# Performance work log

Hardware: AMD Instinct MI355X
Metric: run time of the kernel (lower is better)

The kernel has to match this reference:

```python
import jax, jax.numpy as jnp
import numpy as np

N_NODES = 100000
N_EDGES = 1200000
N_GRAPHS = 256
IN_C, HID_C, OUT_C = 5, 64, 2


def gcn_conv(x, src, dst, W, b, n_nodes):
    """PyG GCNConv: h = x@W; add self-loops; deg from target col (edge weight 1);
    norm = deg^{-1/2}[src]*deg^{-1/2}[dst]; scatter-add messages into dst; + bias."""
    loop = jnp.arange(n_nodes, dtype=src.dtype)
    s = jnp.concatenate([src, loop])
    d = jnp.concatenate([dst, loop])
    deg = jax.ops.segment_sum(jnp.ones_like(d, dtype=x.dtype), d, num_segments=n_nodes)
    dinv = jnp.where(deg > 0, jax.lax.rsqrt(deg), 0.0)
    norm = dinv[s] * dinv[d]                     # [E+N]
    h = x @ W                                    # [N, out]
    msg = h[s] * norm[:, None]                   # gather + scale  [E+N, out]
    out = jax.ops.segment_sum(msg, d, num_segments=n_nodes)  # scatter-add
    return out + b


def setup_inputs() -> dict:
    key = jax.random.key(0)
    ks = jax.random.split(key, 10)
    x = jax.random.normal(ks[0], (N_NODES, IN_C), dtype=jnp.float32)
    edge_index = jax.random.randint(ks[1], (2, N_EDGES), 0, N_NODES, dtype=jnp.int64)
    batch = jnp.sort(jax.random.randint(ks[2], (N_NODES,), 0, N_GRAPHS, dtype=jnp.int64))
    def glorot(k, fan_in, fan_out):
        lim = np.sqrt(6.0 / (fan_in + fan_out))
        return jax.random.uniform(k, (fan_in, fan_out), jnp.float32, -lim, lim)
    W1 = glorot(ks[3], IN_C, HID_C)
    b1 = jnp.zeros((HID_C,), jnp.float32)
    W2 = glorot(ks[4], HID_C, HID_C)
    b2 = jnp.zeros((HID_C,), jnp.float32)
    Wfc = glorot(ks[5], HID_C, OUT_C)
    bfc = jnp.zeros((OUT_C,), jnp.float32)
    return {"x": x, "edge_index": edge_index, "batch": batch,
            "W1": W1, "b1": b1, "W2": W2, "b2": b2, "Wfc": Wfc, "bfc": bfc}


def reference(x, edge_index, batch, W1, b1, W2, b2, Wfc, bfc):
    src, dst = edge_index[0], edge_index[1]
    h = jax.nn.relu(gcn_conv(x, src, dst, W1, b1, N_NODES))
    h = jax.nn.relu(gcn_conv(h, src, dst, W2, b2, N_NODES))
    # global_mean_pool over graph ids in `batch`
    sums = jax.ops.segment_sum(h, batch, num_segments=N_GRAPHS)          # [G, H]
    cnts = jax.ops.segment_sum(jnp.ones((h.shape[0],), h.dtype), batch,
                               num_segments=N_GRAPHS)                    # [G]
    pooled = sums / jnp.maximum(cnts, 1.0)[:, None]
    return pooled @ Wfc + bfc                                            # [G, 2]
```

## Files before the change

### kernel.cpp

```cpp
#include <hip/hip_runtime.h>

#define N_NODES 100000
#define N_EDGES 1200000
#define N_GRAPHS 256
#define IN_C 5
#define HID_C 64
#define OUT_C 2

#define BSH 7
#define BNODES 128
#define NB ((N_NODES + BNODES - 1) / BNODES)
#define CAPB 2048
#define EPB 2048
#define NBLK_E ((N_EDGES + EPB - 1) / EPB)
#define GNPW 8
#define G1NPW 4

typedef unsigned int uint32;

__device__ __forceinline__ uint32 f2bf(float f) {
    uint32 x = __float_as_uint(f);
    return (x + 0x7FFFu + ((x >> 16) & 1u)) >> 16;
}
__device__ __forceinline__ float bflo(uint32 r) { return __uint_as_float(r << 16); }
__device__ __forceinline__ float bfhi(uint32 r) { return __uint_as_float(r & 0xFFFF0000u); }

__global__ void k_bscatter(const int* __restrict__ src, const int* __restrict__ dst,
                           int* __restrict__ bcnt, int* __restrict__ pairs) {
    __shared__ int h[NB];
    for (int i = threadIdx.x; i < NB; i += blockDim.x) h[i] = 0;
    __syncthreads();
    int e0 = blockIdx.x * EPB;
    int e1 = e0 + EPB; if (e1 > N_EDGES) e1 = N_EDGES;
    for (int e = e0 + threadIdx.x; e < e1; e += blockDim.x)
        atomicAdd(&h[dst[e] >> BSH], 1);
    __syncthreads();
    for (int i = threadIdx.x; i < NB; i += blockDim.x)
        if (h[i]) h[i] = (i << 11) + atomicAdd(&bcnt[i], h[i]);
    __syncthreads();
    for (int e = e0 + threadIdx.x; e < e1; e += blockDim.x) {
        int d = dst[e];
        int pos = atomicAdd(&h[d >> BSH], 1);
        pairs[pos] = ((d & (BNODES - 1)) << 17) | src[e];
    }
}

__global__ void k_bsort_g1(const int* __restrict__ pairs, const int* __restrict__ bcnt,
                           const float* __restrict__ x, const float* __restrict__ W1,
                           int* __restrict__ csr, int* __restrict__ rs,
                           int* __restrict__ cnt, float* __restrict__ dinv,
                           uint32* __restrict__ g) {
    __shared__ int hist[BNODES];
    __shared__ int tmp[BNODES];
    __shared__ int cur[BNODES];
    __shared__ float sdv[BNODES];
    __shared__ __align__(16) float sW1[IN_C * HID_C];
    __shared__ float sx[BNODES * IN_C];
    int b = blockIdx.x;
    int t = threadIdx.x;
    int base = b << BSH;
    if (t < BNODES) hist[t] = 0;
    for (int i = t; i < IN_C * HID_C; i += 256) sW1[i] = W1[i];
    for (int i = t; i < BNODES * IN_C; i += 256) {
        int gi = base * IN_C + i;
        sx[i] = (gi < N_NODES * IN_C) ? x[gi] : 0.f;
    }
    __syncthreads();
    int s = b << 11;
    int n = bcnt[b];
    for (int i = t; i < n; i += 256)
        atomicAdd(&hist[pairs[s + i] >> 17], 1);
    __syncthreads();
    int v = (t < BNODES) ? hist[t] : 0;
    if (t < BNODES) tmp[t] = v;
    __syncthreads();
    for (int off = 1; off < BNODES; off <<= 1) {
        int a = (t < BNODES && t >= off) ? tmp[t - off] : 0;
        __syncthreads();
        if (t < BNODES) tmp[t] += a;
        __syncthreads();
    }
    float dv_t = rsqrtf((float)v + 1.0f);
    if (t < BNODES) {
        cur[t] = tmp[t] - v;
        sdv[t] = dv_t;
        if (base + t < N_NODES) {
            rs[base + t] = s + tmp[t] - v;
            cnt[base + t] = v;
            dinv[base + t] = dv_t;
        }
    }
    __syncthreads();
    for (int i = t; i < n; i += 256) {
        int p = pairs[s + i];
        int pos = atomicAdd(&cur[p >> 17], 1);
        csr[s + pos] = p & 0x1FFFF;
    }
    for (int idx = t; idx < BNODES * 32; idx += 256) {
        int nl = idx >> 5, c2 = idx & 31;
        int node = base + nl;
        if (node >= N_NODES) break;
        float s0 = 0.f, s1 = 0.f;
#pragma unroll
        for (int k = 0; k < IN_C; ++k) {
            float xv = sx[nl * IN_C + k];
            float2 wv = *(const float2*)&sW1[k * HID_C + 2 * c2];
            s0 += xv * wv.x;
            s1 += xv * wv.y;
        }
        float dv = sdv[nl];
        g[(unsigned)node * 32 + c2] = (f2bf(s1 * dv) << 16) | f2bf(s0 * dv);
    }
}

__global__ void __launch_bounds__(256) k_gather_g2(
        const uint32* __restrict__ g1t, const int* __restrict__ csr,
        const int* __restrict__ rs, const int* __restrict__ cnt,
        const float* __restrict__ dinv, const float* __restrict__ b1,
        const float* __restrict__ W2, uint32* __restrict__ g2t) {
    __shared__ __align__(16) float sW2[HID_C * HID_C];
    __shared__ float srow[4][HID_C];
    int tid = threadIdx.x;
    for (int i = tid; i < HID_C * HID_C; i += 256) sW2[i] = W2[i];
    __syncthreads();
    int w = tid >> 6;
    int wv = __builtin_amdgcn_readfirstlane(blockIdx.x * 4 + w);
    int n0 = wv * G1NPW;
    if (n0 >= N_NODES) return;
    int n1 = n0 + G1NPW; if (n1 > N_NODES) n1 = N_NODES;
    int lane = tid & 63;
    int half = lane >> 5;
    int c2 = lane & 31;
    float bias0 = b1[2 * c2], bias1 = b1[2 * c2 + 1];
    for (int v = n0; v < n1; ++v) {
        int k0 = rs[v];
        int n = cnt[v];
        float s0 = 0.f, s1 = 0.f;
        if (half == 0) {
            uint32 r = g1t[(unsigned)v * 32 + c2];
            s0 = bflo(r); s1 = bfhi(r);
        }
        int i = 0;
        for (; i + 7 < n; i += 8) {
            int u0 = csr[k0 + i + 0], u1 = csr[k0 + i + 1];
            int u2 = csr[k0 + i + 2], u3 = csr[k0 + i + 3];
            int u4 = csr[k0 + i + 4], u5 = csr[k0 + i + 5];
            int u6 = csr[k0 + i + 6], u7 = csr[k0 + i + 7];
            int a0 = half ? u1 : u0;
            int a1 = half ? u3 : u2;
            int a2 = half ? u5 : u4;
            int a3 = half ? u7 : u6;
            uint32 r0 = g1t[(unsigned)a0 * 32 + c2];
            uint32 r1 = g1t[(unsigned)a1 * 32 + c2];
            uint32 r2 = g1t[(unsigned)a2 * 32 + c2];
            uint32 r3 = g1t[(unsigned)a3 * 32 + c2];
            s0 += (bflo(r0) + bflo(r1)) + (bflo(r2) + bflo(r3));
            s1 += (bfhi(r0) + bfhi(r1)) + (bfhi(r2) + bfhi(r3));
        }
        for (; i + 1 < n; i += 2) {
            int u0 = csr[k0 + i], u1 = csr[k0 + i + 1];
            int a = half ? u1 : u0;
            uint32 r = g1t[(unsigned)a * 32 + c2];
            s0 += bflo(r); s1 += bfhi(r);
        }
        if (i < n && half == 0) {
            uint32 r = g1t[(unsigned)csr[k0 + i] * 32 + c2];
            s0 += bflo(r); s1 += bfhi(r);
        }
        s0 += __shfl_xor(s0, 32);
        s1 += __shfl_xor(s1, 32);
        float dv = dinv[v];
        float o0 = fmaxf(s0 * dv + bias0, 0.f);
        float o1 = fmaxf(s1 * dv + bias1, 0.f);
        if (half == 0) *(float2*)&srow[w][2 * c2] = make_float2(o0, o1);
        int kb = half << 5;
        float a0 = 0.f, a1 = 0.f;
#pragma unroll 8
        for (int j = 0; j < 32; ++j) {
            float hv = srow[w][kb + j];
            float2 wvv = *(const float2*)&sW2[(kb + j) * HID_C + 2 * c2];
            a0 += hv * wvv.x;
            a1 += hv * wvv.y;
        }
        a0 += __shfl_xor(a0, 32);
        a1 += __shfl_xor(a1, 32);
        if (half == 0)
            g2t[(unsigned)v * 32 + c2] = (f2bf(a1 * dv) << 16) | f2bf(a0 * dv);
    }
}

__global__ void k_gather2p(const uint32* __restrict__ g, const int* __restrict__ csr,
                           const int* __restrict__ rs, const int* __restrict__ cnt,
                           const float* __restrict__ dinv, const float* __restrict__ b,
                           const int* __restrict__ batch, float* __restrict__ pooled) {
    int wv = __builtin_amdgcn_readfirstlane(
        blockIdx.x * (blockDim.x >> 6) + (threadIdx.x >> 6));
    int n0 = wv * GNPW;
    if (n0 >= N_NODES) return;
    int n1 = n0 + GNPW; if (n1 > N_NODES) n1 = N_NODES;
    int lane = threadIdx.x & 63;
    int half = lane >> 5;
    int c2 = lane & 31;
    float bias0 = b[2 * c2], bias1 = b[2 * c2 + 1];
    float p0 = 0.f, p1 = 0.f;
    int curg = batch[n0];
    for (int v = n0; v < n1; ++v) {
        int k0 = rs[v];
        int n = cnt[v];
        float s0 = 0.f, s1 = 0.f;
        if (half == 0) {
            uint32 r = g[(unsigned)v * 32 + c2];
            s0 = bflo(r); s1 = bfhi(r);
        }
        int i = 0;
        for (; i + 7 < n; i += 8) {
            int u0 = csr[k0 + i + 0], u1 = csr[k0 + i + 1];
            int u2 = csr[k0 + i + 2], u3 = csr[k0 + i + 3];
            int u4 = csr[k0 + i + 4], u5 = csr[k0 + i + 5];
            int u6 = csr[k0 + i + 6], u7 = csr[k0 + i + 7];
            int a0 = half ? u1 : u0;
            int a1 = half ? u3 : u2;
            int a2 = half ? u5 : u4;
            int a3 = half ? u7 : u6;
            uint32 r0 = g[(unsigned)a0 * 32 + c2];
            uint32 r1 = g[(unsigned)a1 * 32 + c2];
            uint32 r2 = g[(unsigned)a2 * 32 + c2];
            uint32 r3 = g[(unsigned)a3 * 32 + c2];
            s0 += (bflo(r0) + bflo(r1)) + (bflo(r2) + bflo(r3));
            s1 += (bfhi(r0) + bfhi(r1)) + (bfhi(r2) + bfhi(r3));
        }
        for (; i + 1 < n; i += 2) {
            int u0 = csr[k0 + i], u1 = csr[k0 + i + 1];
            int a = half ? u1 : u0;
            uint32 r = g[(unsigned)a * 32 + c2];
            s0 += bflo(r); s1 += bfhi(r);
        }
        if (i < n && half == 0) {
            uint32 r = g[(unsigned)csr[k0 + i] * 32 + c2];
            s0 += bflo(r); s1 += bfhi(r);
        }
        s0 += __shfl_xor(s0, 32);
        s1 += __shfl_xor(s1, 32);
        float dv = dinv[v];
        float o0 = fmaxf(s0 * dv + bias0, 0.f);
        float o1 = fmaxf(s1 * dv + bias1, 0.f);
        int gg = batch[v];
        if (gg != curg) {
            if (half == 0) {
                atomicAdd(&pooled[curg * HID_C + 2 * c2], p0);
                atomicAdd(&pooled[curg * HID_C + 2 * c2 + 1], p1);
            }
            p0 = 0.f; p1 = 0.f; curg = gg;
        }
        p0 += o0; p1 += o1;
    }
    if (half == 0) {
        atomicAdd(&pooled[curg * HID_C + 2 * c2], p0);
        atomicAdd(&pooled[curg * HID_C + 2 * c2 + 1], p1);
    }
}

__global__ void k_fc(const float* __restrict__ pooled, const int* __restrict__ batch,
                     const float* __restrict__ Wfc, const float* __restrict__ bfc,
                     float* __restrict__ out) {
    int g = blockIdx.x;
    int c = threadIdx.x;
    int lo = 0, hi = N_NODES;
    while (lo < hi) { int mid = (lo + hi) >> 1; if (batch[mid] < g) lo = mid + 1; else hi = mid; }
    int start = lo;
    hi = N_NODES;
    while (lo < hi) { int mid = (lo + hi) >> 1; if (batch[mid] < g + 1) lo = mid + 1; else hi = mid; }
    int n = lo - start;
    float pv = pooled[g * HID_C + c] / (float)(n > 0 ? n : 1);
    float o0 = pv * Wfc[c * OUT_C + 0];
    float o1 = pv * Wfc[c * OUT_C + 1];
#pragma unroll
    for (int off = 32; off > 0; off >>= 1) {
        o0 += __shfl_down(o0, off);
        o1 += __shfl_down(o1, off);
    }
    if (c == 0) {
        out[g * OUT_C + 0] = o0 + bfc[0];
        out[g * OUT_C + 1] = o1 + bfc[1];
    }
}

extern "C" void kernel_launch(void* const* d_in, const int* in_sizes, int n_in,
                              void* d_out, int out_size, void* d_ws, size_t ws_size,
                              hipStream_t stream) {
    const float* x    = (const float*)d_in[0];
    const int*   ei   = (const int*)d_in[1];
    const int*   src  = ei;
    const int*   dst  = ei + N_EDGES;
    const int*   batch= (const int*)d_in[2];
    const float* W1   = (const float*)d_in[3];
    const float* b1   = (const float*)d_in[4];
    const float* W2   = (const float*)d_in[5];
    const float* b2   = (const float*)d_in[6];
    const float* Wfc  = (const float*)d_in[7];
    const float* bfc  = (const float*)d_in[8];
    float* out = (float*)d_out;

    float*  ws     = (float*)d_ws;
    int*    bcnt   = (int*)ws;
    float*  pooled = ws + 1024;
    float*  dinv   = pooled + 16384;
    int*    cnt    = (int*)(dinv + 100352);
    int*    rs     = cnt + 100352;
    int*    pairs  = rs + 100352;
    int*    csr    = pairs + (NB * CAPB);
    uint32* g1tab  = (uint32*)(csr + (NB * CAPB));
    uint32* g2tab  = g1tab + N_NODES * 32;

    hipMemsetAsync(bcnt, 0, (1024 + 16384) * sizeof(float), stream);

    k_bscatter<<<NBLK_E, 256, 0, stream>>>(src, dst, bcnt, pairs);
    k_bsort_g1<<<NB, 256, 0, stream>>>(pairs, bcnt, x, W1, csr, rs, cnt, dinv, g1tab);

    {
        int waves = (N_NODES + G1NPW - 1) / G1NPW;
        int blocks = (waves + 3) / 4;
        k_gather_g2<<<blocks, 256, 0, stream>>>(g1tab, csr, rs, cnt, dinv, b1, W2, g2tab);
    }

    {
        int waves = (N_NODES + GNPW - 1) / GNPW;
        int blocks = (waves + 3) / 4;
        k_gather2p<<<blocks, 256, 0, stream>>>(g2tab, csr, rs, cnt, dinv, b2, batch, pooled);
    }

    k_fc<<<N_GRAPHS, 64, 0, stream>>>(pooled, batch, Wfc, bfc, out);
}
```

Before: 222.7 us.

## Pad CSR rows to multiples of four with self-loop and zero sentinel, vectorize gathers

Each CSR row now holds the self-loop and is padded to a multiple of four entries with a sentinel node whose feature row is zero. The gather kernels can then load four indices with one int4 load and have each quarter-wave fetch a uint2 (4 bf16 channels) per neighbor, with no scalar tail loops. The per-bucket CSR capacity is doubled to hold the padding. This removes tail handling and halves the number of feature-load instructions, at the cost of extra sentinel loads, more CSR memory traffic and an added shuffle reduction stage.

```diff
diff --git a/kernel.cpp b/kernel.cpp
--- a/kernel.cpp
+++ b/kernel.cpp
@@ -10,11 +10,13 @@
 #define BSH 7
 #define BNODES 128
 #define NB ((N_NODES + BNODES - 1) / BNODES)
-#define CAPB 2048
+#define CSH 12
+#define CAPB 4096
 #define EPB 2048
 #define NBLK_E ((N_EDGES + EPB - 1) / EPB)
 #define GNPW 8
 #define G1NPW 4
+#define SENT N_NODES
 
 typedef unsigned int uint32;
 
@@ -36,7 +38,7 @@
         atomicAdd(&h[dst[e] >> BSH], 1);
     __syncthreads();
     for (int i = threadIdx.x; i < NB; i += blockDim.x)
-        if (h[i]) h[i] = (i << 11) + atomicAdd(&bcnt[i], h[i]);
+        if (h[i]) h[i] = (i << CSH) + atomicAdd(&bcnt[i], h[i]);
     __syncthreads();
     for (int e = e0 + threadIdx.x; e < e1; e += blockDim.x) {
         int d = dst[e];
@@ -65,14 +67,16 @@
         int gi = base * IN_C + i;
         sx[i] = (gi < N_NODES * IN_C) ? x[gi] : 0.f;
     }
-    __syncthreads();
-    int s = b << 11;
+    if (b == 0 && t < 32) g[(unsigned)SENT * 32 + t] = 0u;
+    __syncthreads();
+    int s = b << CSH;
     int n = bcnt[b];
     for (int i = t; i < n; i += 256)
         atomicAdd(&hist[pairs[s + i] >> 17], 1);
     __syncthreads();
     int v = (t < BNODES) ? hist[t] : 0;
-    if (t < BNODES) tmp[t] = v;
+    int M = (v + 4) & ~3;
+    if (t < BNODES) tmp[t] = M;
     __syncthreads();
     for (int off = 1; off < BNODES; off <<= 1) {
         int a = (t < BNODES && t >= off) ? tmp[t - off] : 0;
@@ -82,11 +86,11 @@
     }
     float dv_t = rsqrtf((float)v + 1.0f);
     if (t < BNODES) {
-        cur[t] = tmp[t] - v;
+        cur[t] = tmp[t] - M;
         sdv[t] = dv_t;
         if (base + t < N_NODES) {
-            rs[base + t] = s + tmp[t] - v;
-            cnt[base + t] = v;
+            rs[base + t] = s + tmp[t] - M;
+            cnt[base + t] = M;
             dinv[base + t] = dv_t;
         }
     }
@@ -95,6 +99,13 @@
         int p = pairs[s + i];
         int pos = atomicAdd(&cur[p >> 17], 1);
         csr[s + pos] = p & 0x1FFFF;
+    }
+    __syncthreads();
+    if (t < BNODES && base + t < N_NODES) {
+        int p0 = cur[t];
+        int pe = tmp[t];
+        csr[s + p0] = base + t;
+        for (int j = p0 + 1; j < pe; ++j) csr[s + j] = SENT;
     }
     for (int idx = t; idx < BNODES * 32; idx += 256) {
         int nl = idx >> 5, c2 = idx & 31;
@@ -122,6 +133,7 @@
     __shared__ float srow[4][HID_C];
     int tid = threadIdx.x;
     for (int i = tid; i < HID_C * HID_C; i += 256) sW2[i] = W2[i];
+    if (blockIdx.x == 0 && tid < 32) g2t[(unsigned)SENT * 32 + tid] = 0u;
     __syncthreads();
     int w = tid >> 6;
     int wv = __builtin_amdgcn_readfirstlane(blockIdx.x * 4 + w);
@@ -129,50 +141,44 @@
     if (n0 >= N_NODES) return;
     int n1 = n0 + G1NPW; if (n1 > N_NODES) n1 = N_NODES;
     int lane = tid & 63;
+    int q = lane >> 4;
+    int c4 = lane & 15;
     int half = lane >> 5;
     int c2 = lane & 31;
-    float bias0 = b1[2 * c2], bias1 = b1[2 * c2 + 1];
+    float4 bia = *(const float4*)&b1[4 * c4];
     for (int v = n0; v < n1; ++v) {
         int k0 = rs[v];
-        int n = cnt[v];
-        float s0 = 0.f, s1 = 0.f;
-        if (half == 0) {
-            uint32 r = g1t[(unsigned)v * 32 + c2];
-            s0 = bflo(r); s1 = bfhi(r);
-        }
+        int M = cnt[v];
+        float s0 = 0.f, s1 = 0.f, s2 = 0.f, s3 = 0.f;
         int i = 0;
-        for (; i + 7 < n; i += 8) {
-            int u0 = csr[k0 + i + 0], u1 = csr[k0 + i + 1];
-            int u2 = csr[k0 + i + 2], u3 = csr[k0 + i + 3];
-            int u4 = csr[k0 + i + 4], u5 = csr[k0 + i + 5];
-            int u6 = csr[k0 + i + 6], u7 = csr[k0 + i + 7];
-            int a0 = half ? u1 : u0;
-            int a1 = half ? u3 : u2;
-            int a2 = half ? u5 : u4;
-            int a3 = half ? u7 : u6;
-            uint32 r0 = g1t[(unsigned)a0 * 32 + c2];
-            uint32 r1 = g1t[(unsigned)a1 * 32 + c2];
-            uint32 r2 = g1t[(unsigned)a2 * 32 + c2];
-            uint32 r3 = g1t[(unsigned)a3 * 32 + c2];
-            s0 += (bflo(r0) + bflo(r1)) + (bflo(r2) + bflo(r3));
-            s1 += (bfhi(r0) + bfhi(r1)) + (bfhi(r2) + bfhi(r3));
-        }
-        for (; i + 1 < n; i += 2) {
-            int u0 = csr[k0 + i], u1 = csr[k0 + i + 1];
-            int a = half ? u1 : u0;
-            uint32 r = g1t[(unsigned)a * 32 + c2];
-            s0 += bflo(r); s1 += bfhi(r);
-        }
-        if (i < n && half == 0) {
-            uint32 r = g1t[(unsigned)csr[k0 + i] * 32 + c2];
-            s0 += bflo(r); s1 += bfhi(r);
-        }
-        s0 += __shfl_xor(s0, 32);
-        s1 += __shfl_xor(s1, 32);
+        for (; i + 8 <= M; i += 8) {
+            int4 ua = *(const int4*)&csr[k0 + i];
+            int4 ub = *(const int4*)&csr[k0 + i + 4];
+            int a0 = (q == 0) ? ua.x : (q == 1) ? ua.y : (q == 2) ? ua.z : ua.w;
+            int a1 = (q == 0) ? ub.x : (q == 1) ? ub.y : (q == 2) ? ub.z : ub.w;
+            uint2 r0 = *(const uint2*)&g1t[(unsigned)a0 * 32 + 2 * c4];
+            uint2 r1 = *(const uint2*)&g1t[(unsigned)a1 * 32 + 2 * c4];
+            s0 += bflo(r0.x) + bflo(r1.x);
+            s1 += bfhi(r0.x) + bfhi(r1.x);
+            s2 += bflo(r0.y) + bflo(r1.y);
+            s3 += bfhi(r0.y) + bfhi(r1.y);
+        }
+        if (i < M) {
+            int4 ua = *(const int4*)&csr[k0 + i];
+            int a0 = (q == 0) ? ua.x : (q == 1) ? ua.y : (q == 2) ? ua.z : ua.w;
+            uint2 r0 = *(const uint2*)&g1t[(unsigned)a0 * 32 + 2 * c4];
+            s0 += bflo(r0.x); s1 += bfhi(r0.x); s2 += bflo(r0.y); s3 += bfhi(r0.y);
+        }
+        s0 += __shfl_xor(s0, 16); s1 += __shfl_xor(s1, 16);
+        s2 += __shfl_xor(s2, 16); s3 += __shfl_xor(s3, 16);
+        s0 += __shfl_xor(s0, 32); s1 += __shfl_xor(s1, 32);
+        s2 += __shfl_xor(s2, 32); s3 += __shfl_xor(s3, 32);
         float dv = dinv[v];
-        float o0 = fmaxf(s0 * dv + bias0, 0.f);
-        float o1 = fmaxf(s1 * dv + bias1, 0.f);
-        if (half == 0) *(float2*)&srow[w][2 * c2] = make_float2(o0, o1);
+        float o0 = fmaxf(s0 * dv + bia.x, 0.f);
+        float o1 = fmaxf(s1 * dv + bia.y, 0.f);
+        float o2 = fmaxf(s2 * dv + bia.z, 0.f);
+        float o3 = fmaxf(s3 * dv + bia.w, 0.f);
+        if (lane < 16) *(float4*)&srow[w][4 * lane] = make_float4(o0, o1, o2, o3);
         int kb = half << 5;
         float a0 = 0.f, a1 = 0.f;
 #pragma unroll 8
@@ -199,64 +205,60 @@
     if (n0 >= N_NODES) return;
     int n1 = n0 + GNPW; if (n1 > N_NODES) n1 = N_NODES;
     int lane = threadIdx.x & 63;
-    int half = lane >> 5;
-    int c2 = lane & 31;
-    float bias0 = b[2 * c2], bias1 = b[2 * c2 + 1];
-    float p0 = 0.f, p1 = 0.f;
+    int q = lane >> 4;
+    int c4 = lane & 15;
+    float4 bia = *(const float4*)&b[4 * c4];
+    float p0 = 0.f, p1 = 0.f, p2 = 0.f, p3 = 0.f;
     int curg = batch[n0];
     for (int v = n0; v < n1; ++v) {
         int k0 = rs[v];
-        int n = cnt[v];
-        float s0 = 0.f, s1 = 0.f;
-        if (half == 0) {
-            uint32 r = g[(unsigned)v * 32 + c2];
-            s0 = bflo(r); s1 = bfhi(r);
-        }
+        int M = cnt[v];
+        float s0 = 0.f, s1 = 0.f, s2 = 0.f, s3 = 0.f;
         int i = 0;
-        for (; i + 7 < n; i += 8) {
-            int u0 = csr[k0 + i + 0], u1 = csr[k0 + i + 1];
-            int u2 = csr[k0 + i + 2], u3 = csr[k0 + i + 3];
-            int u4 = csr[k0 + i + 4], u5 = csr[k0 + i + 5];
-            int u6 = csr[k0 + i + 6], u7 = csr[k0 + i + 7];
-            int a0 = half ? u1 : u0;
-            int a1 = half ? u3 : u2;
-            int a2 = half ? u5 : u4;
-            int a3 = half ? u7 : u6;
-            uint32 r0 = g[(unsigned)a0 * 32 + c2];
-            uint32 r1 = g[(unsigned)a1 * 32 + c2];
-            uint32 r2 = g[(unsigned)a2 * 32 + c2];
-            uint32 r3 = g[(unsigned)a3 * 32 + c2];
-            s0 += (bflo(r0) + bflo(r1)) + (bflo(r2) + bflo(r3));
-            s1 += (bfhi(r0) + bfhi(r1)) + (bfhi(r2) + bfhi(r3));
-        }
-        for (; i + 1 < n; i += 2) {
-            int u0 = csr[k0 + i], u1 = csr[k0 + i + 1];
-            int a = half ? u1 : u0;
-            uint32 r = g[(unsigned)a * 32 + c2];
-            s0 += bflo(r); s1 += bfhi(r);
-        }
-        if (i < n && half == 0) {
-            uint32 r = g[(unsigned)csr[k0 + i] * 32 + c2];
-            s0 += bflo(r); s1 += bfhi(r);
-        }
-        s0 += __shfl_xor(s0, 32);
-        s1 += __shfl_xor(s1, 32);
+        for (; i + 8 <= M; i += 8) {
+            int4 ua = *(const int4*)&csr[k0 + i];
+            int4 ub = *(const int4*)&csr[k0 + i + 4];
+            int a0 = (q == 0) ? ua.x : (q == 1) ? ua.y : (q == 2) ? ua.z : ua.w;
+            int a1 = (q == 0) ? ub.x : (q == 1) ? ub.y : (q == 2) ? ub.z : ub.w;
+            uint2 r0 = *(const uint2*)&g[(unsigned)a0 * 32 + 2 * c4];
+            uint2 r1 = *(const uint2*)&g[(unsigned)a1 * 32 + 2 * c4];
+            s0 += bflo(r0.x) + bflo(r1.x);
+            s1 += bfhi(r0.x) + bfhi(r1.x);
+            s2 += bflo(r0.y) + bflo(r1.y);
+            s3 += bfhi(r0.y) + bfhi(r1.y);
+        }
+        if (i < M) {
+            int4 ua = *(const int4*)&csr[k0 + i];
+            int a0 = (q == 0) ? ua.x : (q == 1) ? ua.y : (q == 2) ? ua.z : ua.w;
+            uint2 r0 = *(const uint2*)&g[(unsigned)a0 * 32 + 2 * c4];
+            s0 += bflo(r0.x); s1 += bfhi(r0.x); s2 += bflo(r0.y); s3 += bfhi(r0.y);
+        }
+        s0 += __shfl_xor(s0, 16); s1 += __shfl_xor(s1, 16);
+        s2 += __shfl_xor(s2, 16); s3 += __shfl_xor(s3, 16);
+        s0 += __shfl_xor(s0, 32); s1 += __shfl_xor(s1, 32);
+        s2 += __shfl_xor(s2, 32); s3 += __shfl_xor(s3, 32);
         float dv = dinv[v];
-        float o0 = fmaxf(s0 * dv + bias0, 0.f);
-        float o1 = fmaxf(s1 * dv + bias1, 0.f);
+        float o0 = fmaxf(s0 * dv + bia.x, 0.f);
+        float o1 = fmaxf(s1 * dv + bia.y, 0.f);
+        float o2 = fmaxf(s2 * dv + bia.z, 0.f);
+        float o3 = fmaxf(s3 * dv + bia.w, 0.f);
         int gg = batch[v];
         if (gg != curg) {
-            if (half == 0) {
-                atomicAdd(&pooled[curg * HID_C + 2 * c2], p0);
-                atomicAdd(&pooled[curg * HID_C + 2 * c2 + 1], p1);
+            if (lane < 16) {
+                atomicAdd(&pooled[curg * HID_C + 4 * c4 + 0], p0);
+                atomicAdd(&pooled[curg * HID_C + 4 * c4 + 1], p1);
+                atomicAdd(&pooled[curg * HID_C + 4 * c4 + 2], p2);
+                atomicAdd(&pooled[curg * HID_C + 4 * c4 + 3], p3);
             }
-            p0 = 0.f; p1 = 0.f; curg = gg;
-        }
-        p0 += o0; p1 += o1;
-    }
-    if (half == 0) {
-        atomicAdd(&pooled[curg * HID_C + 2 * c2], p0);
-        atomicAdd(&pooled[curg * HID_C + 2 * c2 + 1], p1);
+            p0 = p1 = p2 = p3 = 0.f; curg = gg;
+        }
+        p0 += o0; p1 += o1; p2 += o2; p3 += o3;
+    }
+    if (lane < 16) {
+        atomicAdd(&pooled[curg * HID_C + 4 * c4 + 0], p0);
+        atomicAdd(&pooled[curg * HID_C + 4 * c4 + 1], p1);
+        atomicAdd(&pooled[curg * HID_C + 4 * c4 + 2], p2);
+        atomicAdd(&pooled[curg * HID_C + 4 * c4 + 3], p3);
     }
 }
 
@@ -310,7 +312,7 @@
     int*    pairs  = rs + 100352;
     int*    csr    = pairs + (NB * CAPB);
     uint32* g1tab  = (uint32*)(csr + (NB * CAPB));
-    uint32* g2tab  = g1tab + N_NODES * 32;
+    uint32* g2tab  = g1tab + (N_NODES + 1) * 32;
 
     hipMemsetAsync(bcnt, 0, (1024 + 16384) * sizeof(float), stream);
 
```

Result: no change. 224.4 us (+0.8%).
